# Performance work log

Measured on AMD Instinct MI355X. Metric: run time of the kernel, lower is better.

Reference implementation:

```python
import jax, jax.numpy as jnp
import numpy as np

B, S, D = 2, 2048, 512
H, DK, DV = 8, 64, 64
TEMP = DK ** 0.5


def setup_inputs() -> dict:
    key = jax.random.key(0)
    ks = jax.random.split(key, 12)
    inp = {
        "q": jax.random.normal(ks[0], (B, S, D), dtype=jnp.float32),
        "k": jax.random.normal(ks[1], (B, S, D), dtype=jnp.float32),
        "v": jax.random.normal(ks[2], (B, S, D), dtype=jnp.float32),
        "static_cov": jax.random.normal(ks[3], (B, S, S), dtype=jnp.float32),
        "mask": jax.random.randint(ks[4], (B, S, S), 0, 2, dtype=jnp.int32),
        # learned params (torch Linear(bias=False) weight is [out,in]; we store [in,out])
        "w_q": jax.random.normal(ks[5], (D, H * DK), dtype=jnp.float32) / np.sqrt(D),
        "w_k": jax.random.normal(ks[6], (D, H * DK), dtype=jnp.float32) / np.sqrt(D),
        "w_v": jax.random.normal(ks[7], (D, H * DV), dtype=jnp.float32) / np.sqrt(D),
        "w_fc": jax.random.normal(ks[8], (H * DV, D), dtype=jnp.float32) / np.sqrt(H * DV),
        "lambda_w": 10.0 * jnp.ones((1, H, 1, 1), dtype=jnp.float32),
        "ln_gamma": jnp.ones((D,), dtype=jnp.float32),
        "ln_beta": jnp.zeros((D,), dtype=jnp.float32),
    }
    return inp


def reference(q, k, v, static_cov, mask, w_q, w_k, w_v, w_fc, lambda_w, ln_gamma, ln_beta):
    residual = q
    # LayerNorm(eps=1e-6) on q only
    mu = jnp.mean(q, axis=-1, keepdims=True)
    var = jnp.mean(jnp.square(q - mu), axis=-1, keepdims=True)
    qn = (q - mu) / jnp.sqrt(var + 1e-6) * ln_gamma + ln_beta
    # projections -> [B, H, S, d]
    qh = (qn @ w_q).reshape(B, S, H, DK).transpose(0, 2, 1, 3)
    kh = (k @ w_k).reshape(B, S, H, DK).transpose(0, 2, 1, 3)
    vh = (v @ w_v).reshape(B, S, H, DV).transpose(0, 2, 1, 3)
    # convex blend of QK^T and static bias
    scores = jnp.einsum('bhqd,bhkd->bhqk', qh / TEMP, kh)  # [B,H,S,S]
    attn = scores / (lambda_w + 1.0) + (lambda_w / (lambda_w + 1.0)) * static_cov[:, None]
    attn = jnp.where(mask[:, None] == 0, -1e9, attn)
    attn = jax.nn.softmax(attn, axis=-1)
    out = jnp.einsum('bhqk,bhkd->bhqd', attn, vh)
    out = out.transpose(0, 2, 1, 3).reshape(B, S, H * DV)
    out = out @ w_fc + residual
    return (out, attn)
```

## Files before the change

kernel.cpp:

```cpp
#include <hip/hip_runtime.h>
#include <hip/hip_bf16.h>

typedef __attribute__((ext_vector_type(4))) float f32x4;
typedef __attribute__((ext_vector_type(4))) int i32x4;
typedef __attribute__((ext_vector_type(4))) unsigned int u32x4;
typedef __attribute__((ext_vector_type(8))) __bf16 bf16x8;

#define SDIM 2048
#define DDIM 512
#define HH 8
#define DH 64

static __device__ __forceinline__ f32x4 mfma_raw(bf16x8 a, bf16x8 b, f32x4 c) {
  return __builtin_amdgcn_mfma_f32_16x16x32_bf16(a, b, c, 0, 0, 0);
}

template <bool C1>
static __device__ __forceinline__ f32x4 mf(bf16x8 a, bf16x8 b, f32x4 c) {
  return C1 ? mfma_raw(a, b, c) : mfma_raw(b, a, c);
}

static __device__ __forceinline__ unsigned pack_bf16(float a, float b) {
  __bf16 x = (__bf16)a, y = (__bf16)b;
  unsigned short ux = __builtin_bit_cast(unsigned short, x);
  unsigned short uy = __builtin_bit_cast(unsigned short, y);
  return ((unsigned)uy << 16) | (unsigned)ux;
}

__global__ __launch_bounds__(256) void stageA_kernel(const float* __restrict__ cov,
                                                     const int* __restrict__ mask,
                                                     float* __restrict__ covm,
                                                     const float* __restrict__ q,
                                                     const float* __restrict__ gamma,
                                                     const float* __restrict__ beta,
                                                     __bf16* __restrict__ qn,
                                                     const float* __restrict__ w0,
                                                     const float* __restrict__ w1,
                                                     const float* __restrict__ w2,
                                                     const float* __restrict__ w3,
                                                     __bf16* __restrict__ t0,
                                                     __bf16* __restrict__ t1,
                                                     __bf16* __restrict__ t2,
                                                     __bf16* __restrict__ t3,
                                                     int* __restrict__ flag) {
  __shared__ float tile[64][65];
  int bid = blockIdx.x;
  if (bid < 8192) {
    size_t i = ((size_t)bid * 256 + threadIdx.x) * 4;
    f32x4 c = *(const f32x4*)(cov + i);
    i32x4 m = *(const i32x4*)(mask + i);
    f32x4 o;
#pragma unroll
    for (int r = 0; r < 4; ++r) o[r] = (m[r] == 0) ? -1e38f : c[r];
    *(f32x4*)(covm + i) = o;
    return;
  }
  if (bid < 9216) {
    int lb = bid - 8192;
    if (lb == 0 && threadIdx.x < 64) {
      float av = (float)(threadIdx.x & 15);
      float bv = av * av;
      bf16x8 a, b;
#pragma unroll
      for (int i = 0; i < 8; ++i) { a[i] = (__bf16)av; b[i] = (__bf16)bv; }
      f32x4 d = {};
      d = mfma_raw(a, b, d);
      if (threadIdx.x == 17) *flag = (d[0] == 128.0f) ? 1 : 2;
    }
    int row = lb * 4 + (threadIdx.x >> 6);
    int lane = threadIdx.x & 63;
    const float* qr = q + (size_t)row * DDIM + lane * 8;
    f32x4 x0 = *(const f32x4*)qr;
    f32x4 x1 = *(const f32x4*)(qr + 4);
    float s = 0.f;
#pragma unroll
    for (int i = 0; i < 4; ++i) s += x0[i] + x1[i];
#pragma unroll
    for (int off = 32; off; off >>= 1) s += __shfl_xor(s, off);
    float mu = s * (1.f / DDIM);
    float vs = 0.f;
#pragma unroll
    for (int i = 0; i < 4; ++i) {
      float d0 = x0[i] - mu, d1 = x1[i] - mu;
      vs += d0 * d0 + d1 * d1;
    }
#pragma unroll
    for (int off = 32; off; off >>= 1) vs += __shfl_xor(vs, off);
    float inv = rsqrtf(vs * (1.f / DDIM) + 1e-6f);
    const float* g = gamma + lane * 8;
    const float* be = beta + lane * 8;
    bf16x8 o;
#pragma unroll
    for (int i = 0; i < 8; ++i) {
      float xv = (i < 4) ? x0[i] : x1[i - 4];
      o[i] = (__bf16)((xv - mu) * inv * g[i] + be[i]);
    }
    *(bf16x8*)(qn + (size_t)row * DDIM + lane * 8) = o;
    return;
  }
  int wb = bid - 9216;
  int which = wb >> 6;
  int rem = wb & 63;
  int n0 = (rem & 7) * 64;
  int k0 = (rem >> 3) * 64;
  const float* w = which == 0 ? w0 : which == 1 ? w1 : which == 2 ? w2 : w3;
  __bf16* t = which == 0 ? t0 : which == 1 ? t1 : which == 2 ? t2 : t3;
  int tx = threadIdx.x & 63, ty = threadIdx.x >> 6;
#pragma unroll
  for (int j = 0; j < 16; ++j) {
    int kk = ty * 16 + j;
    tile[kk][tx] = w[(size_t)(k0 + kk) * DDIM + n0 + tx];
  }
  __syncthreads();
#pragma unroll
  for (int j = 0; j < 16; ++j) {
    int n = ty * 16 + j;
    t[(size_t)(n0 + n) * DDIM + k0 + tx] = (__bf16)tile[tx][n];
  }
}

template <bool C1>
static __device__ __forceinline__ void proj_body(const __bf16* __restrict__ qn,
                                                 const float* __restrict__ kin,
                                                 const float* __restrict__ vin,
                                                 const __bf16* __restrict__ wqT,
                                                 const __bf16* __restrict__ wkT,
                                                 const __bf16* __restrict__ wvT,
                                                 const float* __restrict__ lam,
                                                 __bf16* __restrict__ qh,
                                                 __bf16* __restrict__ kh,
                                                 __bf16* __restrict__ vT,
                                                 __bf16* __restrict__ tr) {
  int which = blockIdx.z;
  int n0 = blockIdx.x * 64;
  int m0 = blockIdx.y * 64;
  int wid = threadIdx.x >> 6, lane = threadIdx.x & 63;
  int lr = lane & 15, lg = lane >> 4;
  int mrow = m0 + wid * 16;
  const __bf16* wT = which == 0 ? wqT : which == 1 ? wkT : wvT;
  f32x4 acc[4] = {};
  for (int kb = 0; kb < DDIM; kb += 32) {
    bf16x8 afrag;
    if (which == 0) {
      afrag = *(const bf16x8*)(qn + (size_t)(mrow + lr) * DDIM + kb + lg * 8);
    } else {
      const float* src = (which == 1 ? kin : vin) + (size_t)(mrow + lr) * DDIM + kb + lg * 8;
      f32x4 y0 = *(const f32x4*)src;
      f32x4 y1 = *(const f32x4*)(src + 4);
#pragma unroll
      for (int i = 0; i < 4; ++i) { afrag[i] = (__bf16)y0[i]; afrag[i + 4] = (__bf16)y1[i]; }
    }
#pragma unroll
    for (int c = 0; c < 4; ++c) {
      bf16x8 bfrag = *(const bf16x8*)(wT + (size_t)(n0 + c * 16 + lr) * DDIM + kb + lg * 8);
      acc[c] = mf<C1>(afrag, bfrag, acc[c]);
    }
  }
  int h = n0 >> 6;
  int bq = m0 >> 11;
  int ss0 = m0 & 2047;
  if (which == 0) {
    float sc = 1.f / (8.f * (lam[h] + 1.f));
#pragma unroll
    for (int c = 0; c < 4; ++c)
#pragma unroll
      for (int r = 0; r < 4; ++r)
        tr[(wid * 16 + lg * 4 + r) * 72 + c * 16 + lr] = (__bf16)(acc[c][r] * sc);
  } else if (which == 1) {
#pragma unroll
    for (int c = 0; c < 4; ++c)
#pragma unroll
      for (int r = 0; r < 4; ++r)
        tr[(wid * 16 + lg * 4 + r) * 72 + c * 16 + lr] = (__bf16)acc[c][r];
  } else {
#pragma unroll
    for (int c = 0; c < 4; ++c)
#pragma unroll
      for (int r = 0; r < 4; ++r)
        tr[(c * 16 + lr) * 72 + wid * 16 + lg * 4 + r] = (__bf16)acc[c][r];
  }
  __syncthreads();
  size_t bh2 = (size_t)bq * HH + h;
#pragma unroll
  for (int ii = 0; ii < 2; ++ii) {
    int row = (threadIdx.x >> 3) + ii * 32;
    int col = (threadIdx.x & 7) * 8;
    bf16x8 v8 = *(const bf16x8*)(tr + row * 72 + col);
    if (which == 2) {
      *(bf16x8*)(vT + (bh2 * DH + row) * SDIM + ss0 + col) = v8;
    } else {
      __bf16* dst = (which == 0 ? qh : kh);
      *(bf16x8*)(dst + (bh2 * SDIM + ss0 + row) * DH + col) = v8;
    }
  }
}

__global__ __launch_bounds__(256) void proj_kernel(const __bf16* __restrict__ qn,
                                                   const float* __restrict__ kin,
                                                   const float* __restrict__ vin,
                                                   const __bf16* __restrict__ wqT,
                                                   const __bf16* __restrict__ wkT,
                                                   const __bf16* __restrict__ wvT,
                                                   const float* __restrict__ lam,
                                                   __bf16* __restrict__ qh,
                                                   __bf16* __restrict__ kh,
                                                   __bf16* __restrict__ vT,
                                                   const int* __restrict__ flag) {
  extern __shared__ __bf16 psm[];
  if (*flag == 1) proj_body<true>(qn, kin, vin, wqT, wkT, wvT, lam, qh, kh, vT, psm);
  else            proj_body<false>(qn, kin, vin, wqT, wkT, wvT, lam, qh, kh, vT, psm);
}

template <bool C1>
static __device__ __forceinline__ void fused_body(const __bf16* __restrict__ qh,
                                                  const __bf16* __restrict__ kh,
                                                  const __bf16* __restrict__ vT,
                                                  const float* __restrict__ covm,
                                                  const float* __restrict__ lam,
                                                  float* __restrict__ attn,
                                                  __bf16* __restrict__ oh,
                                                  float* __restrict__ smem) {
  float* part  = smem;
  float* wredm = smem + 8 * 64 * 17;
  float* wreds = wredm + 128;
  int bid = blockIdx.x;
  int xcd = bid & 7;
  int seq = bid >> 3;
  int bh  = xcd * 2 + (seq & 1);
  int q0  = (seq >> 1) * 16;
  int b = bh >> 3, h = bh & 7;
  int wid = threadIdx.x >> 6, lane = threadIdx.x & 63;
  int lr = lane & 15, lg = lane >> 4;
  int col0 = wid * 256;
  const __bf16* qbase = qh + ((size_t)bh * SDIM + q0) * DH;
  const __bf16* kbase = kh + (size_t)bh * SDIM * DH;
  bf16x8 qf0 = *(const bf16x8*)(qbase + lr * DH + lg * 8);
  bf16x8 qf1 = *(const bf16x8*)(qbase + lr * DH + 32 + lg * 8);
  f32x4 acc[16];
#pragma unroll
  for (int c = 0; c < 16; ++c) {
    const __bf16* kp = kbase + (size_t)(col0 + c * 16 + lr) * DH + lg * 8;
    bf16x8 k0 = *(const bf16x8*)kp;
    bf16x8 k1 = *(const bf16x8*)(kp + 32);
    f32x4 t = {};
    t = mf<C1>(k0, qf0, t);
    t = mf<C1>(k1, qf1, t);
    acc[c] = t;
  }
  float blend = lam[h] / (lam[h] + 1.f);
  const float* crow = covm + ((size_t)b * SDIM + q0 + lr) * SDIM + col0 + lg * 4;
  float mx = -3.4e38f;
#pragma unroll
  for (int c = 0; c < 16; ++c) {
    f32x4 cv = *(const f32x4*)(crow + c * 16);
#pragma unroll
    for (int r = 0; r < 4; ++r) {
      float valv = acc[c][r] + blend * cv[r];
      valv = (cv[r] < -1e30f) ? -1e9f : valv;
      acc[c][r] = valv;
      mx = fmaxf(mx, valv);
    }
  }
  mx = fmaxf(mx, __shfl_xor(mx, 16));
  mx = fmaxf(mx, __shfl_xor(mx, 32));
  float sm = 0.f;
#pragma unroll
  for (int c = 0; c < 16; ++c) {
#pragma unroll
    for (int r = 0; r < 4; ++r) {
      float p = __expf(acc[c][r] - mx);
      acc[c][r] = p;
      sm += p;
    }
  }
  sm += __shfl_xor(sm, 16);
  sm += __shfl_xor(sm, 32);
  if (lg == 0) {
    wredm[wid * 16 + lr] = mx;
    wreds[wid * 16 + lr] = sm;
  }
  __syncthreads();
  float M = wredm[lr];
#pragma unroll
  for (int w = 1; w < 8; ++w) M = fmaxf(M, wredm[w * 16 + lr]);
  float denom = 0.f;
#pragma unroll
  for (int w = 0; w < 8; ++w) denom += wreds[w * 16 + lr] * __expf(wredm[w * 16 + lr] - M);
  float sc = __expf(mx - M) / denom;
  const __bf16* vbase = vT + (size_t)bh * DH * SDIM + col0;
  int src0 = lr + 32 * (lg & 1);
  int src1 = src0 + 16;
  bool hi = (lg & 2) != 0;
  f32x4 oacc[4] = {};
#pragma unroll
  for (int t = 0; t < 8; ++t) {
    unsigned p0 = pack_bf16(acc[t * 2][0], acc[t * 2][1]);
    unsigned p1 = pack_bf16(acc[t * 2][2], acc[t * 2][3]);
    unsigned p2 = pack_bf16(acc[t * 2 + 1][0], acc[t * 2 + 1][1]);
    unsigned p3 = pack_bf16(acc[t * 2 + 1][2], acc[t * 2 + 1][3]);
    unsigned a0 = (unsigned)__shfl((int)p0, src0);
    unsigned a1 = (unsigned)__shfl((int)p1, src0);
    unsigned b0 = (unsigned)__shfl((int)p2, src0);
    unsigned b1 = (unsigned)__shfl((int)p3, src0);
    unsigned a2 = (unsigned)__shfl((int)p0, src1);
    unsigned a3 = (unsigned)__shfl((int)p1, src1);
    unsigned b2 = (unsigned)__shfl((int)p2, src1);
    unsigned b3 = (unsigned)__shfl((int)p3, src1);
    u32x4 wv;
    wv[0] = hi ? b0 : a0;
    wv[1] = hi ? b1 : a1;
    wv[2] = hi ? b2 : a2;
    wv[3] = hi ? b3 : a3;
    bf16x8 pfrag = __builtin_bit_cast(bf16x8, wv);
#pragma unroll
    for (int cp = 0; cp < 4; ++cp) {
      bf16x8 vfrag = *(const bf16x8*)(vbase + (size_t)(cp * 16 + lr) * SDIM + t * 32 + lg * 8);
      oacc[cp] = mf<C1>(vfrag, pfrag, oacc[cp]);
    }
  }
#pragma unroll
  for (int cp = 0; cp < 4; ++cp)
#pragma unroll
    for (int rp = 0; rp < 4; ++rp)
      part[(wid * 64 + cp * 16 + lg * 4 + rp) * 17 + lr] = oacc[cp][rp] * sc;
  __syncthreads();
  float* abase = attn + ((size_t)bh * SDIM + q0 + lr) * SDIM + col0 + lg * 4;
#pragma unroll
  for (int c = 0; c < 16; ++c) {
    f32x4 pn;
#pragma unroll
    for (int r = 0; r < 4; ++r) pn[r] = acc[c][r] * sc;
    *(f32x4*)(abase + c * 16) = pn;
  }
  {
    int qq = threadIdx.x >> 5;
    int dv = (threadIdx.x & 31) * 2;
    float s0 = 0.f, s1 = 0.f;
#pragma unroll
    for (int w = 0; w < 8; ++w) {
      s0 += part[(w * 64 + dv) * 17 + qq];
      s1 += part[(w * 64 + dv + 1) * 17 + qq];
    }
    unsigned ow = pack_bf16(s0, s1);
    *(unsigned*)(oh + ((size_t)(b * SDIM + q0 + qq)) * DDIM + h * DH + dv) = ow;
  }
}

__global__ __launch_bounds__(512, 4) void fused_kernel_cov(const __bf16* __restrict__ qh,
                                                           const __bf16* __restrict__ kh,
                                                           const __bf16* __restrict__ vT,
                                                           const float* __restrict__ covm,
                                                           const float* __restrict__ lam,
                                                           float* __restrict__ attn,
                                                           __bf16* __restrict__ oh,
                                                           const int* __restrict__ flag) {
  extern __shared__ float smem[];
  if (*flag == 1) fused_body<true>(qh, kh, vT, covm, lam, attn, oh, smem);
  else            fused_body<false>(qh, kh, vT, covm, lam, attn, oh, smem);
}

template <bool C1>
static __device__ __forceinline__ void fc_body(const __bf16* __restrict__ oh,
                                               const __bf16* __restrict__ wfcT,
                                               const float* __restrict__ resid,
                                               float* __restrict__ out) {
  int n0 = blockIdx.x * 64;
  int m0 = blockIdx.y * 64;
  int wid = threadIdx.x >> 6, lane = threadIdx.x & 63;
  int lr = lane & 15, lg = lane >> 4;
  int mrow = m0 + wid * 16;
  f32x4 acc[4] = {};
  for (int kb = 0; kb < DDIM; kb += 32) {
    bf16x8 afrag = *(const bf16x8*)(oh + (size_t)(mrow + lr) * DDIM + kb + lg * 8);
#pragma unroll
    for (int c = 0; c < 4; ++c) {
      bf16x8 bfrag = *(const bf16x8*)(wfcT + (size_t)(n0 + c * 16 + lr) * DDIM + kb + lg * 8);
      acc[c] = mf<C1>(afrag, bfrag, acc[c]);
    }
  }
#pragma unroll
  for (int c = 0; c < 4; ++c)
#pragma unroll
    for (int r = 0; r < 4; ++r) {
      size_t m = mrow + lg * 4 + r;
      size_t n = n0 + c * 16 + lr;
      out[m * DDIM + n] = acc[c][r] + resid[m * DDIM + n];
    }
}

__global__ __launch_bounds__(256) void fc_kernel(const __bf16* __restrict__ oh,
                                                 const __bf16* __restrict__ wfcT,
                                                 const float* __restrict__ resid,
                                                 float* __restrict__ out,
                                                 const int* __restrict__ flag) {
  if (*flag == 1) fc_body<true>(oh, wfcT, resid, out);
  else            fc_body<false>(oh, wfcT, resid, out);
}

extern "C" void kernel_launch(void* const* d_in, const int* in_sizes, int n_in,
                              void* d_out, int out_size, void* d_ws, size_t ws_size,
                              hipStream_t stream) {
  const float* q = (const float*)d_in[0];
  const float* k = (const float*)d_in[1];
  const float* v = (const float*)d_in[2];
  const float* static_cov = (const float*)d_in[3];
  const int* mask = (const int*)d_in[4];
  const float* w_q = (const float*)d_in[5];
  const float* w_k = (const float*)d_in[6];
  const float* w_v = (const float*)d_in[7];
  const float* w_fc = (const float*)d_in[8];
  const float* lam = (const float*)d_in[9];
  const float* gamma = (const float*)d_in[10];
  const float* beta = (const float*)d_in[11];

  float* out = (float*)d_out;
  float* attn = out + (size_t)2 * SDIM * DDIM;

  char* ws = (char*)d_ws;
  const size_t MB4 = (size_t)4 << 20;
  __bf16* qn  = (__bf16*)(ws);
  __bf16* qh  = (__bf16*)(ws + 1 * MB4);
  __bf16* kh  = (__bf16*)(ws + 2 * MB4);
  __bf16* vT  = (__bf16*)(ws + 3 * MB4);
  __bf16* oh  = (__bf16*)(ws + 4 * MB4);
  __bf16* wqT = (__bf16*)(ws + 5 * MB4);
  __bf16* wkT = (__bf16*)(ws + 5 * MB4 + 524288);
  __bf16* wvT = (__bf16*)(ws + 5 * MB4 + 2 * 524288);
  __bf16* wfcT= (__bf16*)(ws + 5 * MB4 + 3 * 524288);
  int* flag   = (int*)(ws + 5 * MB4 + 4 * 524288);
  float* covm = (float*)(ws + 6 * MB4);

  const unsigned fused_smem = (8 * 64 * 17 + 128 + 128) * 4;
  const unsigned proj_smem  = 64 * 72 * 2;

  stageA_kernel<<<dim3(9472), dim3(256), 0, stream>>>(static_cov, mask, covm,
                                                      q, gamma, beta, qn,
                                                      w_q, w_k, w_v, w_fc,
                                                      wqT, wkT, wvT, wfcT, flag);
  proj_kernel<<<dim3(8, 64, 3), dim3(256), proj_smem, stream>>>(qn, k, v, wqT, wkT, wvT, lam, qh, kh, vT, flag);
  fused_kernel_cov<<<dim3(2048), dim3(512), fused_smem, stream>>>(qh, kh, vT, covm, lam, attn, oh, flag);
  fc_kernel<<<dim3(8, 64), dim3(256), 0, stream>>>(oh, wfcT, q, out, flag);
}
```

Baseline: 299.9 us.

## Store masked static covariance as bf16 in a fragment-permuted layout

The pre-pass that folds the mask into the static covariance now writes bf16 instead of fp32. It also permutes elements within each 256-column chunk so every lane of the fused attention kernel can fetch its 16 values with two 16-byte loads instead of 16-byte fp32 loads per column tile. This halves the intermediate buffer's write and read traffic and cuts load instruction count. The cost is bf16 rounding of the static bias, which is scaled by about 0.9 before softmax and may reduce accuracy of the attention output.

```diff
diff --git a/kernel.cpp b/kernel.cpp
--- a/kernel.cpp
+++ b/kernel.cpp
@@ -5,6 +5,7 @@
 typedef __attribute__((ext_vector_type(4))) int i32x4;
 typedef __attribute__((ext_vector_type(4))) unsigned int u32x4;
 typedef __attribute__((ext_vector_type(8))) __bf16 bf16x8;
+typedef __attribute__((ext_vector_type(4))) __bf16 bf16x4;
 
 #define SDIM 2048
 #define DDIM 512
@@ -29,7 +30,7 @@
 
 __global__ __launch_bounds__(256) void stageA_kernel(const float* __restrict__ cov,
                                                      const int* __restrict__ mask,
-                                                     float* __restrict__ covm,
+                                                     __bf16* __restrict__ covm,
                                                      const float* __restrict__ q,
                                                      const float* __restrict__ gamma,
                                                      const float* __restrict__ beta,
@@ -49,10 +50,14 @@
     size_t i = ((size_t)bid * 256 + threadIdx.x) * 4;
     f32x4 c = *(const f32x4*)(cov + i);
     i32x4 m = *(const i32x4*)(mask + i);
-    f32x4 o;
-#pragma unroll
-    for (int r = 0; r < 4; ++r) o[r] = (m[r] == 0) ? -1e38f : c[r];
-    *(f32x4*)(covm + i) = o;
+    unsigned o = (unsigned)(i & 255);
+    unsigned c16 = o >> 4;
+    unsigned lgp = (o >> 2) & 3;
+    size_t dst = (i & ~(size_t)255) + lgp * 64 + c16 * 4;
+    bf16x4 ob;
+#pragma unroll
+    for (int r = 0; r < 4; ++r) ob[r] = (__bf16)((m[r] == 0) ? -1e38f : c[r]);
+    *(bf16x4*)(covm + dst) = ob;
     return;
   }
   if (bid < 9216) {
@@ -215,7 +220,7 @@
 static __device__ __forceinline__ void fused_body(const __bf16* __restrict__ qh,
                                                   const __bf16* __restrict__ kh,
                                                   const __bf16* __restrict__ vT,
-                                                  const float* __restrict__ covm,
+                                                  const __bf16* __restrict__ covm,
                                                   const float* __restrict__ lam,
                                                   float* __restrict__ attn,
                                                   __bf16* __restrict__ oh,
@@ -248,15 +253,18 @@
     acc[c] = t;
   }
   float blend = lam[h] / (lam[h] + 1.f);
-  const float* crow = covm + ((size_t)b * SDIM + q0 + lr) * SDIM + col0 + lg * 4;
+  const __bf16* crow = covm + ((size_t)b * SDIM + q0 + lr) * SDIM + col0 + lg * 64;
   float mx = -3.4e38f;
 #pragma unroll
-  for (int c = 0; c < 16; ++c) {
-    f32x4 cv = *(const f32x4*)(crow + c * 16);
-#pragma unroll
-    for (int r = 0; r < 4; ++r) {
-      float valv = acc[c][r] + blend * cv[r];
-      valv = (cv[r] < -1e30f) ? -1e9f : valv;
+  for (int cc = 0; cc < 8; ++cc) {
+    bf16x8 cv = *(const bf16x8*)(crow + cc * 8);
+#pragma unroll
+    for (int j = 0; j < 8; ++j) {
+      int c = cc * 2 + (j >> 2);
+      int r = j & 3;
+      float cf = (float)cv[j];
+      float valv = acc[c][r] + blend * cf;
+      valv = (cf < -1e30f) ? -1e9f : valv;
       acc[c][r] = valv;
       mx = fmaxf(mx, valv);
     }
@@ -349,7 +357,7 @@
 __global__ __launch_bounds__(512, 4) void fused_kernel_cov(const __bf16* __restrict__ qh,
                                                            const __bf16* __restrict__ kh,
                                                            const __bf16* __restrict__ vT,
-                                                           const float* __restrict__ covm,
+                                                           const __bf16* __restrict__ covm,
                                                            const float* __restrict__ lam,
                                                            float* __restrict__ attn,
                                                            __bf16* __restrict__ oh,
@@ -428,7 +436,7 @@
   __bf16* wvT = (__bf16*)(ws + 5 * MB4 + 2 * 524288);
   __bf16* wfcT= (__bf16*)(ws + 5 * MB4 + 3 * 524288);
   int* flag   = (int*)(ws + 5 * MB4 + 4 * 524288);
-  float* covm = (float*)(ws + 6 * MB4);
+  __bf16* covm = (__bf16*)(ws + 6 * MB4);
 
   const unsigned fused_smem = (8 * 64 * 17 + 128 + 128) * 4;
   const unsigned proj_smem  = 64 * 72 * 2;
```

Result: faster. 284.7 us (-5.1%).
